# Optimization experiments

Hardware: AMD Instinct MI355X
Metric: run time of the kernel (lower is better)

## Reference

```python
import jax, jax.numpy as jnp
import numpy as np

B, N, C = 4, 8192, 512
H, Dh, G, R = 8, 64, 64, 2  # heads, dim_head, slice_num, mlp_ratio
EPS_LN = 1e-5
EPS_NORM = 1e-5


def _ln(x, g, b):
    m = jnp.mean(x, axis=-1, keepdims=True)
    v = jnp.var(x, axis=-1, keepdims=True)
    return (x - m) * jax.lax.rsqrt(v + EPS_LN) * g + b


def setup_inputs() -> dict:
    key = jax.random.key(0)
    ks = jax.random.split(key, 16)
    r = lambda k, shp: jax.random.normal(k, shp, jnp.float32) * 0.02
    inner = H * Dh
    return {
        "fx": jax.random.normal(ks[0], (B, N, C), jnp.float32),
        "ln1_g": jnp.ones((C,), jnp.float32), "ln1_b": jnp.zeros((C,), jnp.float32),
        "Wx": r(ks[1], (C, inner)), "bx": jnp.zeros((inner,), jnp.float32),
        "Wfx": r(ks[2], (C, inner)), "bfx": jnp.zeros((inner,), jnp.float32),
        "Wslice": r(ks[3], (Dh, G)), "bslice": jnp.zeros((G,), jnp.float32),
        "temperature": jnp.full((1, H, 1, 1), 0.5, jnp.float32),
        "Wq": r(ks[4], (Dh, Dh)), "Wk": r(ks[5], (Dh, Dh)), "Wv": r(ks[6], (Dh, Dh)),
        "Wout": r(ks[7], (inner, C)), "bout": jnp.zeros((C,), jnp.float32),
        "tln_g": jnp.ones((Dh,), jnp.float32), "tln_b": jnp.zeros((Dh,), jnp.float32),
        "Wm1": r(ks[8], (Dh, R * Dh)), "bm1": jnp.zeros((R * Dh,), jnp.float32),
        "Wm2": r(ks[9], (R * Dh, Dh)), "bm2": jnp.zeros((Dh,), jnp.float32),
    }


def reference(fx, ln1_g, ln1_b, Wx, bx, Wfx, bfx, Wslice, bslice, temperature,
              Wq, Wk, Wv, Wout, bout, tln_g, tln_b, Wm1, bm1, Wm2, bm2):
    fx_norm = _ln(fx, ln1_g, ln1_b)                          # [B,N,C]
    # _forward_slice: project to per-head mid features
    x_mid = (fx_norm @ Wx + bx).reshape(B, N, H, Dh).transpose(0, 2, 1, 3)   # [B,H,N,Dh]
    fx_mid = (fx_norm @ Wfx + bfx).reshape(B, N, H, Dh).transpose(0, 2, 1, 3)
    # _project_token: soft slice assignment + weighted pooling into G tokens
    logits = jnp.einsum('bhnd,dg->bhng', x_mid, Wslice) + bslice
    slice_w = jax.nn.softmax(logits / temperature, axis=-1)  # [B,H,N,G]
    slice_norm = jnp.sum(slice_w, axis=2)                    # [B,H,G]
    slice_tok = jnp.einsum('bhnd,bhng->bhgd', fx_mid, slice_w) / (slice_norm[..., None] + EPS_NORM)
    # attention over the small token set (G tokens)
    q = slice_tok @ Wq
    k = slice_tok @ Wk
    v = slice_tok @ Wv
    scale = Dh ** -0.5
    attn = jax.nn.softmax(jnp.einsum('bhgd,bhpd->bhgp', q, k) * scale, axis=-1)
    out_tok = jnp.einsum('bhgp,bhpd->bhgd', attn, v) + slice_tok
    # token MLP with residual
    h = _ln(out_tok, tln_g, tln_b)
    h = jax.nn.gelu(h @ Wm1 + bm1, approximate=False) @ Wm2 + bm2
    tokens = h + out_tok                                     # [B,H,G,Dh]
    # _deslice: weighted scatter back to N points, merge heads, out projection
    out_x = jnp.einsum('bhgd,bhng->bhnd', tokens, slice_w)
    out_x = out_x.transpose(0, 2, 1, 3).reshape(B, N, H * Dh)
    out = out_x @ Wout + bout
    return out + fx_norm
```

## Files before the change

### kernel.cpp

```cpp
#include <hip/hip_runtime.h>
#include <math.h>

#define B_ 4
#define N_ 8192
#define C_ 512
#define H_ 8
#define M_ (B_ * N_)

typedef __attribute__((ext_vector_type(8))) short bf16x8;
typedef __attribute__((ext_vector_type(4))) float f32x4;
typedef __attribute__((ext_vector_type(8))) unsigned short u16x8;
typedef __attribute__((ext_vector_type(4))) unsigned short u16x4;

__device__ __forceinline__ float b2f(unsigned short u) {
  union { unsigned int i; float f; } v;
  v.i = ((unsigned int)u) << 16;
  return v.f;
}
__device__ __forceinline__ unsigned short f2b(float f) {
  union { float f; unsigned int i; } v;
  v.f = f;
  unsigned int r = v.i + 0x7fff + ((v.i >> 16) & 1);
  return (unsigned short)(r >> 16);
}
__device__ __forceinline__ void gl_lds16(const void* g, void* l) {
  __builtin_amdgcn_global_load_lds(
      (const __attribute__((address_space(1))) unsigned int*)g,
      (__attribute__((address_space(3))) unsigned int*)l, 16, 0, 0);
}

__global__ __launch_bounds__(256) void ln_bf16(
    const float* __restrict__ x, const float* __restrict__ gam,
    const float* __restrict__ bet, unsigned short* __restrict__ y) {
  int wave = threadIdx.x >> 6, lane = threadIdx.x & 63;
  int row = (blockIdx.x << 2) + wave;
  const float4* xr = (const float4*)(x + (size_t)row * C_);
  float4 v0 = xr[lane], v1 = xr[lane + 64];
  float s = v0.x + v0.y + v0.z + v0.w + v1.x + v1.y + v1.z + v1.w;
  float q = v0.x * v0.x + v0.y * v0.y + v0.z * v0.z + v0.w * v0.w +
            v1.x * v1.x + v1.y * v1.y + v1.z * v1.z + v1.w * v1.w;
#pragma unroll
  for (int off = 32; off; off >>= 1) {
    s += __shfl_xor(s, off);
    q += __shfl_xor(q, off);
  }
  float mean = s * (1.0f / C_);
  float var = q * (1.0f / C_) - mean * mean;
  float rstd = rsqrtf(var + 1e-5f);
  const float4* gr = (const float4*)gam;
  const float4* br = (const float4*)bet;
  float4 g0 = gr[lane], g1 = gr[lane + 64];
  float4 b0 = br[lane], b1 = br[lane + 64];
  u16x4 oa, ob;
  oa.x = f2b((v0.x - mean) * rstd * g0.x + b0.x);
  oa.y = f2b((v0.y - mean) * rstd * g0.y + b0.y);
  oa.z = f2b((v0.z - mean) * rstd * g0.z + b0.z);
  oa.w = f2b((v0.w - mean) * rstd * g0.w + b0.w);
  ob.x = f2b((v1.x - mean) * rstd * g1.x + b1.x);
  ob.y = f2b((v1.y - mean) * rstd * g1.y + b1.y);
  ob.z = f2b((v1.z - mean) * rstd * g1.z + b1.z);
  ob.w = f2b((v1.w - mean) * rstd * g1.w + b1.w);
  unsigned short* yr = y + (size_t)row * C_;
  *(u16x4*)(yr + (lane << 2)) = oa;
  *(u16x4*)(yr + 256 + (lane << 2)) = ob;
}

__global__ __launch_bounds__(256) void prep_all(
    const float* __restrict__ Wx, const float* __restrict__ Wfx,
    const float* __restrict__ Wout, const float* __restrict__ Wsl,
    const float* __restrict__ Wq, const float* __restrict__ Wk,
    const float* __restrict__ Wv, const float* __restrict__ Wm1,
    const float* __restrict__ Wm2, unsigned short* __restrict__ WtX,
    unsigned short* __restrict__ WtF, unsigned short* __restrict__ WtO,
    unsigned short* __restrict__ wsf, unsigned short* __restrict__ wfr) {
  __shared__ float tile[64][65];
  int blk = blockIdx.x, t = threadIdx.x;
  if (blk < 192) {
    int which = blk >> 6, sub = blk & 63;
    const float* W = (which == 0) ? Wx : (which == 1) ? Wfx : Wout;
    unsigned short* Wt = (which == 0) ? WtX : (which == 1) ? WtF : WtO;
    int r0 = (sub >> 3) << 6, c0 = (sub & 7) << 6;
    int lr = t >> 4, lc = (t & 15) << 2;
#pragma unroll
    for (int p = 0; p < 4; p++) {
      float4 v = *(const float4*)(W + (size_t)(r0 + lr + p * 16) * 512 + c0 + lc);
      tile[lr + p * 16][lc + 0] = v.x;
      tile[lr + p * 16][lc + 1] = v.y;
      tile[lr + p * 16][lc + 2] = v.z;
      tile[lr + p * 16][lc + 3] = v.w;
    }
    __syncthreads();
    int on = t >> 2, ok = (t & 3) << 4;
    unsigned short tmp[16];
#pragma unroll
    for (int j = 0; j < 16; j++) tmp[j] = f2b(tile[ok + j][on]);
    unsigned short* op = Wt + (size_t)(c0 + on) * 512 + r0 + ok;
#pragma unroll
    for (int j4 = 0; j4 < 4; j4++)
      *(u16x4*)(op + (j4 << 2)) = *(u16x4*)(tmp + (j4 << 2));
  } else {
#pragma unroll
    for (int i = 0; i < 2; i++) {
      int idx = t + i * 256;
      int f = idx >> 6, l = idx & 63;
      int gt = f >> 1, ks = f & 1;
      int g = (gt << 4) + (l & 15);
      int d0 = (ks << 5) + ((l >> 4) << 3);
      unsigned short v[8];
#pragma unroll
      for (int jj = 0; jj < 8; jj++) v[jj] = f2b(Wsl[(size_t)(d0 + jj) * 64 + g]);
      *(u16x4*)(wsf + idx * 8) = *(u16x4*)v;
      *(u16x4*)(wsf + idx * 8 + 4) = *(u16x4*)(v + 4);
    }
    for (int task = t; task < 56 * 64; task += 256) {
      int fid = task >> 6, l = task & 63;
      const float* W;
      int stride, ct, ks;
      if (fid < 24) {
        W = (fid < 8) ? Wq : (fid < 16) ? Wk : Wv;
        int e = fid & 7;
        ct = e >> 1;
        ks = e & 1;
        stride = 64;
      } else if (fid < 40) {
        W = Wm1;
        int e = fid - 24;
        ct = e >> 1;
        ks = e & 1;
        stride = 128;
      } else {
        W = Wm2;
        int e = fid - 40;
        ct = e >> 2;
        ks = e & 3;
        stride = 64;
      }
      int d0 = (ks << 5) + ((l >> 4) << 3);
      int c = (ct << 4) + (l & 15);
      unsigned short v[8];
#pragma unroll
      for (int j = 0; j < 8; j++) v[j] = f2b(W[(size_t)(d0 + j) * stride + c]);
      *(u16x4*)(wfr + task * 8) = *(u16x4*)v;
      *(u16x4*)(wfr + task * 8 + 4) = *(u16x4*)(v + 4);
    }
  }
}

__global__ __launch_bounds__(256) void tokfrag_prep(
    const float* __restrict__ tokens, unsigned short* __restrict__ wtokf) {
  int bh = blockIdx.x, t = threadIdx.x, w = t >> 6, l = t & 63;
  const float* tp = tokens + ((size_t)bh << 12);
#pragma unroll
  for (int fid = w; fid < 8; fid += 4) {
    int mt = fid >> 1, ks = fid & 1;
    int d = (mt << 4) + (l & 15);
    int g0 = (ks << 5) + ((l >> 4) << 3);
    unsigned short v[8];
#pragma unroll
    for (int j = 0; j < 8; j++) v[j] = f2b(tp[(g0 + j) * 64 + d]);
    unsigned short* op = wtokf + (((size_t)bh << 3) + fid) * 512 + (l << 3);
    *(u16x4*)op = *(u16x4*)v;
    *(u16x4*)(op + 4) = *(u16x4*)(v + 4);
  }
}

template <int DEC, bool BIASROW, bool OUTBF, bool RES>
__global__ __launch_bounds__(256) void gemm_bf16(
    const unsigned short* __restrict__ A, const unsigned short* __restrict__ Bt,
    const float* __restrict__ bias, const unsigned short* __restrict__ resid,
    void* __restrict__ Cout, size_t ldC) {
  __shared__ unsigned short lds[8192];
  const int t = threadIdx.x;
  const int w = t >> 6, l = t & 63;
  int bid = blockIdx.x;
  int xcd = bid & 7, q = bid >> 3;
  int bm, bn;
  if (DEC == 0) {
    bm = ((xcd << 5) + (q >> 2)) << 7;
    bn = (q & 3) << 7;
  } else {
    bn = ((xcd << 5) + (q >> 2)) << 7;
    bm = (q & 3) << 7;
  }
  const int wm = (w >> 1) << 6, wn = (w & 1) << 6;
  f32x4 acc[4][4];
#pragma unroll
  for (int mt = 0; mt < 4; mt++)
#pragma unroll
    for (int nt = 0; nt < 4; nt++) acc[mt][nt] = (f32x4){0.f, 0.f, 0.f, 0.f};

  const int srow = t >> 2;
  const int scol = (((t & 3) ^ ((t >> 3) & 3)) << 3);
  const unsigned short* gA0 = A + (size_t)(bm + srow) * 512 + scol;
  const unsigned short* gA1 = A + (size_t)(bm + 64 + srow) * 512 + scol;
  const unsigned short* gB0 = Bt + (size_t)(bn + srow) * 512 + scol;
  const unsigned short* gB1 = Bt + (size_t)(bn + 64 + srow) * 512 + scol;
  const int fr = l & 15;
  const int pslot = (((l >> 4) ^ ((l >> 1) & 3)) << 3);

  for (int k0 = 0; k0 < 512; k0 += 32) {
    gl_lds16(gA0 + k0, lds + (w << 9));
    gl_lds16(gA1 + k0, lds + 2048 + (w << 9));
    gl_lds16(gB0 + k0, lds + 4096 + (w << 9));
    gl_lds16(gB1 + k0, lds + 6144 + (w << 9));
    __syncthreads();
    bf16x8 af[4], bfr[4];
#pragma unroll
    for (int mt = 0; mt < 4; mt++)
      af[mt] = *(const bf16x8*)&lds[(wm + mt * 16 + fr) * 32 + pslot];
#pragma unroll
    for (int nt = 0; nt < 4; nt++)
      bfr[nt] = *(const bf16x8*)&lds[4096 + (wn + nt * 16 + fr) * 32 + pslot];
#pragma unroll
    for (int mt = 0; mt < 4; mt++)
#pragma unroll
      for (int nt = 0; nt < 4; nt++)
        acc[mt][nt] = __builtin_amdgcn_mfma_f32_16x16x32_bf16(
            af[mt], bfr[nt], acc[mt][nt], 0, 0, 0);
    __syncthreads();
  }

  const int col0 = bn + wn + (l & 15);
  const int row0 = bm + wm + ((l >> 4) << 2);
#pragma unroll
  for (int mt = 0; mt < 4; mt++) {
#pragma unroll
    for (int j = 0; j < 4; j++) {
      int row = row0 + mt * 16 + j;
#pragma unroll
      for (int nt = 0; nt < 4; nt++) {
        int col = col0 + nt * 16;
        float v = acc[mt][nt][j] + (BIASROW ? bias[row] : bias[col]);
        if (RES) v += b2f(resid[(size_t)row * ldC + col]);
        if (OUTBF)
          ((unsigned short*)Cout)[(size_t)row * ldC + col] = f2b(v);
        else
          ((float*)Cout)[(size_t)row * ldC + col] = v;
      }
    }
  }
}

__global__ __launch_bounds__(256) void slice_mfma(
    unsigned short* __restrict__ xw, const unsigned short* __restrict__ wf,
    const float* __restrict__ bslice, const float* __restrict__ temp) {
  __shared__ unsigned short xs[4096];
  int t = threadIdx.x, w = t >> 6, l = t & 63;
  int blk = blockIdx.x;
  size_t base = (size_t)blk << 12;
  {
    int srow = t >> 2;
    const unsigned short* gp = xw + base + srow * 64 + ((t & 3) << 4);
    u16x8 a = *(const u16x8*)gp;
    u16x8 b = *(const u16x8*)(gp + 8);
    int sl0 = (t & 3) << 1, swz = srow & 7;
    *(u16x8*)&xs[srow * 64 + ((sl0 ^ swz) << 3)] = a;
    *(u16x8*)&xs[srow * 64 + (((sl0 + 1) ^ swz) << 3)] = b;
  }
  bf16x8 wsf[4][2];
#pragma unroll
  for (int gt = 0; gt < 4; gt++)
#pragma unroll
    for (int ks = 0; ks < 2; ks++)
      wsf[gt][ks] = *(const bf16x8*)(wf + (((gt << 1) + ks) * 64 + l) * 8);
  __syncthreads();

  int xr = (w << 4) + (l & 15);
  f32x4 acc[4];
#pragma unroll
  for (int gt = 0; gt < 4; gt++) acc[gt] = (f32x4){0.f, 0.f, 0.f, 0.f};
#pragma unroll
  for (int ks = 0; ks < 2; ks++) {
    int slot = (ks << 2) + (l >> 4);
    bf16x8 xf = *(const bf16x8*)&xs[xr * 64 + ((slot ^ (xr & 7)) << 3)];
#pragma unroll
    for (int gt = 0; gt < 4; gt++)
      acc[gt] = __builtin_amdgcn_mfma_f32_16x16x32_bf16(wsf[gt][ks], xf,
                                                        acc[gt], 0, 0, 0);
  }

  int gxr = (blk << 6) + xr;
  float invt = 1.0f / temp[gxr & 7];
  int qq = l >> 4;
  float lg[16];
  float mx = -1e30f;
#pragma unroll
  for (int gt = 0; gt < 4; gt++)
#pragma unroll
    for (int r = 0; r < 4; r++) {
      float v = (acc[gt][r] + bslice[(gt << 4) + (qq << 2) + r]) * invt;
      lg[(gt << 2) + r] = v;
      mx = fmaxf(mx, v);
    }
  mx = fmaxf(mx, __shfl_xor(mx, 16));
  mx = fmaxf(mx, __shfl_xor(mx, 32));
  float ssum = 0.f;
#pragma unroll
  for (int i = 0; i < 16; i++) {
    lg[i] = expf(lg[i] - mx);
    ssum += lg[i];
  }
  ssum += __shfl_xor(ssum, 16);
  ssum += __shfl_xor(ssum, 32);
  float inv = 1.0f / ssum;
  __syncthreads();
#pragma unroll
  for (int gt = 0; gt < 4; gt++) {
    int slot = (gt << 1) + (qq >> 1);
    int off = ((slot ^ (xr & 7)) << 3) + ((qq & 1) << 2);
    u16x4 pk;
    pk.x = f2b(lg[(gt << 2) + 0] * inv);
    pk.y = f2b(lg[(gt << 2) + 1] * inv);
    pk.z = f2b(lg[(gt << 2) + 2] * inv);
    pk.w = f2b(lg[(gt << 2) + 3] * inv);
    *(u16x4*)&xs[xr * 64 + off] = pk;
  }
  __syncthreads();
  {
    int rr = (w << 4) + (l >> 2);
    int sl = (l & 3) << 1, swz = rr & 7;
    u16x8 o0 = *(const u16x8*)&xs[rr * 64 + ((sl ^ swz) << 3)];
    u16x8 o1 = *(const u16x8*)&xs[rr * 64 + (((sl + 1) ^ swz) << 3)];
    unsigned short* op = xw + base + rr * 64 + ((l & 3) << 4);
    *(u16x8*)op = o0;
    *(u16x8*)(op + 8) = o1;
  }
}

__global__ __launch_bounds__(256) void pool_mfma(
    const unsigned short* __restrict__ sw, const unsigned short* __restrict__ fxT,
    float* __restrict__ tok_part, float* __restrict__ norm_part) {
  __shared__ unsigned short wT[4096];
  int bid = blockIdx.x;
  int bh = bid >> 4, c = bid & 15;
  int b = bh >> 3, h = bh & 7;
  int t = threadIdx.x, w = t >> 6, l = t & 63;
  int n0 = c << 9;
  const int fr15 = l & 15, fs = l >> 4;
  f32x4 acc[4];
#pragma unroll
  for (int gt = 0; gt < 4; gt++) acc[gt] = (f32x4){0.f, 0.f, 0.f, 0.f};
  float nacc[4] = {0.f, 0.f, 0.f, 0.f};

  const unsigned short* fxrow =
      fxT + (size_t)(h * 64 + w * 16 + fr15) * 32768 + b * N_ + n0 + (fs << 3);

  for (int nn = 0; nn < 512; nn += 64) {
    size_t srow = ((size_t)(b * N_ + n0 + nn + l) * 8 + h) << 6;
    u16x8 a0 = *(const u16x8*)(sw + srow + w * 16);
    u16x8 a1 = *(const u16x8*)(sw + srow + w * 16 + 8);
    __syncthreads();
#pragma unroll
    for (int j = 0; j < 16; j++) {
      int g = (w << 4) + j;
      unsigned short v = (j < 8) ? (unsigned short)a0[j] : (unsigned short)a1[j - 8];
      wT[(g << 6) + (((l >> 3) ^ (g & 7)) << 3) + (l & 7)] = v;
    }
    __syncthreads();
#pragma unroll
    for (int kk = 0; kk < 2; kk++) {
      bf16x8 bfrag = *(const bf16x8*)(fxrow + nn + (kk << 5));
#pragma unroll
      for (int gt = 0; gt < 4; gt++) {
        int g = (gt << 4) + fr15;
        int slot = (kk << 2) + fs;
        bf16x8 af = *(const bf16x8*)&wT[(g << 6) + ((slot ^ (g & 7)) << 3)];
        acc[gt] = __builtin_amdgcn_mfma_f32_16x16x32_bf16(af, bfrag, acc[gt], 0, 0, 0);
        if (w == 0) {
#pragma unroll
          for (int j = 0; j < 8; j++) nacc[gt] += b2f((unsigned short)af[j]);
        }
      }
    }
  }
  float* op = tok_part + ((size_t)bid << 12);
#pragma unroll
  for (int gt = 0; gt < 4; gt++)
#pragma unroll
    for (int rr = 0; rr < 4; rr++)
      op[((gt << 4) + (fs << 2) + rr) * 64 + (w << 4) + fr15] = acc[gt][rr];
  if (w == 0) {
#pragma unroll
    for (int gt = 0; gt < 4; gt++) {
      float s = nacc[gt];
      s += __shfl_xor(s, 16);
      s += __shfl_xor(s, 32);
      if (l < 16) norm_part[(bid << 6) + (gt << 4) + l] = s;
    }
  }
}

__global__ __launch_bounds__(256) void tok_reduce(
    const float* __restrict__ tok_part, const float* __restrict__ norm_part,
    float* __restrict__ stG) {
  int blk = blockIdx.x;
  int bh = blk >> 2, qq = blk & 3;
  int t = threadIdx.x;
  int e = (qq << 10) + (t << 2);
  int g = e >> 6;
  float s = 0.f;
  const float* np = norm_part + ((size_t)bh << 10);
#pragma unroll
  for (int c = 0; c < 16; c++) s += np[(c << 6) + g];
  float4 acc = make_float4(0.f, 0.f, 0.f, 0.f);
  const float* tp = tok_part + ((size_t)bh << 16) + e;
#pragma unroll
  for (int c = 0; c < 16; c++) {
    float4 v = *(const float4*)(tp + (c << 12));
    acc.x += v.x;
    acc.y += v.y;
    acc.z += v.z;
    acc.w += v.w;
  }
  float inv = 1.0f / (s + 1e-5f);
  acc.x *= inv;
  acc.y *= inv;
  acc.z *= inv;
  acc.w *= inv;
  *(float4*)(stG + ((size_t)bh << 12) + e) = acc;
}

__device__ __forceinline__ float gelu_exact(float x) {
  return 0.5f * x * (1.0f + erff(x * 0.70710678118654752f));
}

__global__ __launch_bounds__(256) void token_mfma(
    const float* __restrict__ stG, const unsigned short* __restrict__ wfr,
    const float* __restrict__ tg, const float* __restrict__ tb,
    const float* __restrict__ bm1, const float* __restrict__ bm2,
    float* __restrict__ tokens) {
  __shared__ __align__(16) char smem[54272];
  unsigned short* stb = (unsigned short*)smem;
  float* st32 = (float*)(smem + 9216);
  unsigned short* hmld = (unsigned short*)(smem + 9216);
  unsigned short* qld = (unsigned short*)(smem + 26624);
  unsigned short* kld = (unsigned short*)(smem + 35840);
  unsigned short* vtl = (unsigned short*)(smem + 45056);

  int bh = blockIdx.x, t = threadIdx.x, w = t >> 6, l = t & 63;
  const int fr = l & 15, fq = l >> 4;

  {
    int r = t >> 2, c0 = (t & 3) << 4;
    const float* gp = stG + ((size_t)bh << 12) + r * 64 + c0;
    float4 a = *(const float4*)gp;
    float4 b = *(const float4*)(gp + 4);
    float4 c = *(const float4*)(gp + 8);
    float4 d = *(const float4*)(gp + 12);
    *(float4*)&st32[r * 68 + c0] = a;
    *(float4*)&st32[r * 68 + c0 + 4] = b;
    *(float4*)&st32[r * 68 + c0 + 8] = c;
    *(float4*)&st32[r * 68 + c0 + 12] = d;
    unsigned short tv[16];
    tv[0] = f2b(a.x); tv[1] = f2b(a.y); tv[2] = f2b(a.z); tv[3] = f2b(a.w);
    tv[4] = f2b(b.x); tv[5] = f2b(b.y); tv[6] = f2b(b.z); tv[7] = f2b(b.w);
    tv[8] = f2b(c.x); tv[9] = f2b(c.y); tv[10] = f2b(c.z); tv[11] = f2b(c.w);
    tv[12] = f2b(d.x); tv[13] = f2b(d.y); tv[14] = f2b(d.z); tv[15] = f2b(d.w);
    *(u16x8*)&stb[r * 72 + c0] = *(u16x8*)tv;
    *(u16x8*)&stb[r * 72 + c0 + 8] = *(u16x8*)(tv + 8);
  }
  __syncthreads();

  const int orow = (w << 4) + (fq << 2);

  {
    bf16x8 af[2];
#pragma unroll
    for (int ks = 0; ks < 2; ks++)
      af[ks] = *(const bf16x8*)&stb[((w << 4) + fr) * 72 + (ks << 5) + (fq << 3)];
    f32x4 aq[4], ak[4], av[4];
#pragma unroll
    for (int ct = 0; ct < 4; ct++) {
      aq[ct] = (f32x4){0.f, 0.f, 0.f, 0.f};
      ak[ct] = (f32x4){0.f, 0.f, 0.f, 0.f};
      av[ct] = (f32x4){0.f, 0.f, 0.f, 0.f};
    }
#pragma unroll
    for (int ct = 0; ct < 4; ct++)
#pragma unroll
      for (int ks = 0; ks < 2; ks++) {
        bf16x8 bq = *(const bf16x8*)&wfr[(((ct << 1) + ks) * 64 + l) * 8];
        aq[ct] = __builtin_amdgcn_mfma_f32_16x16x32_bf16(af[ks], bq, aq[ct], 0, 0, 0);
      }
#pragma unroll
    for (int ct = 0; ct < 4; ct++)
#pragma unroll
      for (int ks = 0; ks < 2; ks++) {
        bf16x8 bk = *(const bf16x8*)&wfr[((8 + (ct << 1) + ks) * 64 + l) * 8];
        ak[ct] = __builtin_amdgcn_mfma_f32_16x16x32_bf16(af[ks], bk, ak[ct], 0, 0, 0);
      }
#pragma unroll
    for (int ct = 0; ct < 4; ct++)
#pragma unroll
      for (int ks = 0; ks < 2; ks++) {
        bf16x8 bv = *(const bf16x8*)&wfr[((16 + (ct << 1) + ks) * 64 + l) * 8];
        av[ct] = __builtin_amdgcn_mfma_f32_16x16x32_bf16(af[ks], bv, av[ct], 0, 0, 0);
      }
#pragma unroll
    for (int ct = 0; ct < 4; ct++) {
#pragma unroll
      for (int rr = 0; rr < 4; rr++) {
        qld[(orow + rr) * 72 + (ct << 4) + fr] = f2b(aq[ct][rr]);
        kld[(orow + rr) * 72 + (ct << 4) + fr] = f2b(ak[ct][rr]);
      }
      u16x4 vp;
      vp.x = f2b(av[ct][0]);
      vp.y = f2b(av[ct][1]);
      vp.z = f2b(av[ct][2]);
      vp.w = f2b(av[ct][3]);
      *(u16x4*)&vtl[((ct << 4) + fr) * 72 + orow] = vp;
    }
  }
  __syncthreads();

  {
    bf16x8 aq[2];
#pragma unroll
    for (int ks = 0; ks < 2; ks++)
      aq[ks] = *(const bf16x8*)&qld[((w << 4) + fr) * 72 + (ks << 5) + (fq << 3)];
    f32x4 accs[4];
#pragma unroll
    for (int nt = 0; nt < 4; nt++) accs[nt] = (f32x4){0.f, 0.f, 0.f, 0.f};
#pragma unroll
    for (int nt = 0; nt < 4; nt++)
#pragma unroll
      for (int ks = 0; ks < 2; ks++) {
        bf16x8 bk = *(const bf16x8*)&kld[((nt << 4) + fr) * 72 + (ks << 5) + (fq << 3)];
        accs[nt] = __builtin_amdgcn_mfma_f32_16x16x32_bf16(aq[ks], bk, accs[nt], 0, 0, 0);
      }
#pragma unroll
    for (int rr = 0; rr < 4; rr++) {
      float v0 = accs[0][rr] * 0.125f, v1 = accs[1][rr] * 0.125f;
      float v2 = accs[2][rr] * 0.125f, v3 = accs[3][rr] * 0.125f;
      float mx = fmaxf(fmaxf(v0, v1), fmaxf(v2, v3));
      mx = fmaxf(mx, __shfl_xor(mx, 1));
      mx = fmaxf(mx, __shfl_xor(mx, 2));
      mx = fmaxf(mx, __shfl_xor(mx, 4));
      mx = fmaxf(mx, __shfl_xor(mx, 8));
      float e0 = expf(v0 - mx), e1 = expf(v1 - mx);
      float e2 = expf(v2 - mx), e3 = expf(v3 - mx);
      float ss = e0 + e1 + e2 + e3;
      ss += __shfl_xor(ss, 1);
      ss += __shfl_xor(ss, 2);
      ss += __shfl_xor(ss, 4);
      ss += __shfl_xor(ss, 8);
      float inv = 1.0f / ss;
      stb[(orow + rr) * 72 + 0 * 16 + fr] = f2b(e0 * inv);
      stb[(orow + rr) * 72 + 1 * 16 + fr] = f2b(e1 * inv);
      stb[(orow + rr) * 72 + 2 * 16 + fr] = f2b(e2 * inv);
      stb[(orow + rr) * 72 + 3 * 16 + fr] = f2b(e3 * inv);
    }
  }
  __syncthreads();

  float o16[4][4];
  {
    bf16x8 ap[2];
#pragma unroll
    for (int ks = 0; ks < 2; ks++)
      ap[ks] = *(const bf16x8*)&stb[((w << 4) + fr) * 72 + (ks << 5) + (fq << 3)];
    f32x4 acco[4];
#pragma unroll
    for (int ct = 0; ct < 4; ct++) acco[ct] = (f32x4){0.f, 0.f, 0.f, 0.f};
#pragma unroll
    for (int ct = 0; ct < 4; ct++)
#pragma unroll
      for (int ks = 0; ks < 2; ks++) {
        bf16x8 bv = *(const bf16x8*)&vtl[((ct << 4) + fr) * 72 + (ks << 5) + (fq << 3)];
        acco[ct] = __builtin_amdgcn_mfma_f32_16x16x32_bf16(ap[ks], bv, acco[ct], 0, 0, 0);
      }
    float tgv[4], tbv[4];
#pragma unroll
    for (int ct = 0; ct < 4; ct++) {
      tgv[ct] = tg[(ct << 4) + fr];
      tbv[ct] = tb[(ct << 4) + fr];
    }
#pragma unroll
    for (int ct = 0; ct < 4; ct++)
#pragma unroll
      for (int rr = 0; rr < 4; rr++)
        o16[ct][rr] = acco[ct][rr] + st32[(orow + rr) * 68 + (ct << 4) + fr];
#pragma unroll
    for (int rr = 0; rr < 4; rr++) {
      float sm = o16[0][rr] + o16[1][rr] + o16[2][rr] + o16[3][rr];
      float sq = o16[0][rr] * o16[0][rr] + o16[1][rr] * o16[1][rr] +
                 o16[2][rr] * o16[2][rr] + o16[3][rr] * o16[3][rr];
      sm += __shfl_xor(sm, 1);
      sm += __shfl_xor(sm, 2);
      sm += __shfl_xor(sm, 4);
      sm += __shfl_xor(sm, 8);
      sq += __shfl_xor(sq, 1);
      sq += __shfl_xor(sq, 2);
      sq += __shfl_xor(sq, 4);
      sq += __shfl_xor(sq, 8);
      float mean = sm * (1.0f / 64.0f);
      float var = sq * (1.0f / 64.0f) - mean * mean;
      float rstd = rsqrtf(var + 1e-5f);
#pragma unroll
      for (int ct = 0; ct < 4; ct++) {
        float hv = (o16[ct][rr] - mean) * rstd * tgv[ct] + tbv[ct];
        qld[(orow + rr) * 72 + (ct << 4) + fr] = f2b(hv);
      }
    }
  }
  __syncthreads();

  {
    bf16x8 ah[2];
#pragma unroll
    for (int ks = 0; ks < 2; ks++)
      ah[ks] = *(const bf16x8*)&qld[((w << 4) + fr) * 72 + (ks << 5) + (fq << 3)];
    f32x4 accm[8];
#pragma unroll
    for (int et = 0; et < 8; et++) accm[et] = (f32x4){0.f, 0.f, 0.f, 0.f};
#pragma unroll
    for (int et = 0; et < 8; et++)
#pragma unroll
      for (int ks = 0; ks < 2; ks++) {
        bf16x8 bm = *(const bf16x8*)&wfr[((24 + (et << 1) + ks) * 64 + l) * 8];
        accm[et] = __builtin_amdgcn_mfma_f32_16x16x32_bf16(ah[ks], bm, accm[et], 0, 0, 0);
      }
#pragma unroll
    for (int et = 0; et < 8; et++) {
      float bv = bm1[(et << 4) + fr];
#pragma unroll
      for (int rr = 0; rr < 4; rr++) {
        float x = accm[et][rr] + bv;
        hmld[(orow + rr) * 136 + (et << 4) + fr] = f2b(gelu_exact(x));
      }
    }
  }
  __syncthreads();

  {
    bf16x8 ahm[4];
#pragma unroll
    for (int ks = 0; ks < 4; ks++)
      ahm[ks] = *(const bf16x8*)&hmld[((w << 4) + fr) * 136 + (ks << 5) + (fq << 3)];
    f32x4 acc2[4];
#pragma unroll
    for (int ct = 0; ct < 4; ct++) acc2[ct] = (f32x4){0.f, 0.f, 0.f, 0.f};
#pragma unroll
    for (int ct = 0; ct < 4; ct++)
#pragma unroll
      for (int ks = 0; ks < 4; ks++) {
        bf16x8 bw = *(const bf16x8*)&wfr[((40 + (ct << 2) + ks) * 64 + l) * 8];
        acc2[ct] = __builtin_amdgcn_mfma_f32_16x16x32_bf16(ahm[ks], bw, acc2[ct], 0, 0, 0);
      }
    float* tout = tokens + ((size_t)bh << 12);
#pragma unroll
    for (int ct = 0; ct < 4; ct++) {
      float bv = bm2[(ct << 4) + fr];
#pragma unroll
      for (int rr = 0; rr < 4; rr++)
        tout[(orow + rr) * 64 + (ct << 4) + fr] = acc2[ct][rr] + bv + o16[ct][rr];
    }
  }
}

__global__ __launch_bounds__(256) void deslice_mfma(
    const unsigned short* __restrict__ wtokf, const unsigned short* __restrict__ sw,
    unsigned short* __restrict__ outx) {
  int bid = blockIdx.x;
  int bh = bid >> 4, c = bid & 15;
  int b = bh >> 3, h = bh & 7;
  int t = threadIdx.x, w = t >> 6, l = t & 63;
  const int fr = l & 15, fq = l >> 4;

  bf16x8 ta[4][2];
  const unsigned short* fp = wtokf + ((size_t)bh << 12);
#pragma unroll
  for (int mt = 0; mt < 4; mt++)
#pragma unroll
    for (int ks = 0; ks < 2; ks++)
      ta[mt][ks] = *(const bf16x8*)(fp + (((mt << 1) + ks) << 9) + (l << 3));

  int n0 = (c << 9) + (w << 7);
#pragma unroll 2
  for (int ntile = 0; ntile < 8; ntile++) {
    int nb = n0 + (ntile << 4);
    size_t rowb = ((size_t)(b * N_ + nb + fr) * 8 + h) << 6;
    bf16x8 b0 = *(const bf16x8*)(sw + rowb + (fq << 3));
    bf16x8 b1 = *(const bf16x8*)(sw + rowb + 32 + (fq << 3));
    f32x4 acc[4];
#pragma unroll
    for (int mt = 0; mt < 4; mt++) acc[mt] = (f32x4){0.f, 0.f, 0.f, 0.f};
#pragma unroll
    for (int mt = 0; mt < 4; mt++) {
      acc[mt] = __builtin_amdgcn_mfma_f32_16x16x32_bf16(ta[mt][0], b0, acc[mt], 0, 0, 0);
      acc[mt] = __builtin_amdgcn_mfma_f32_16x16x32_bf16(ta[mt][1], b1, acc[mt], 0, 0, 0);
    }
    unsigned short* op = outx + rowb + (fq << 2);
#pragma unroll
    for (int mt = 0; mt < 4; mt++) {
      u16x4 pk;
      pk.x = f2b(acc[mt][0]);
      pk.y = f2b(acc[mt][1]);
      pk.z = f2b(acc[mt][2]);
      pk.w = f2b(acc[mt][3]);
      *(u16x4*)(op + (mt << 4)) = pk;
    }
  }
}

extern "C" void kernel_launch(void* const* d_in, const int* in_sizes, int n_in,
                              void* d_out, int out_size, void* d_ws,
                              size_t ws_size, hipStream_t stream) {
  const float* fx = (const float*)d_in[0];
  const float* ln1g = (const float*)d_in[1];
  const float* ln1b = (const float*)d_in[2];
  const float* Wx = (const float*)d_in[3];
  const float* bx = (const float*)d_in[4];
  const float* Wfx = (const float*)d_in[5];
  const float* bfx = (const float*)d_in[6];
  const float* Wsl = (const float*)d_in[7];
  const float* bsl = (const float*)d_in[8];
  const float* temp = (const float*)d_in[9];
  const float* Wq = (const float*)d_in[10];
  const float* Wk = (const float*)d_in[11];
  const float* Wv = (const float*)d_in[12];
  const float* Wout = (const float*)d_in[13];
  const float* bout = (const float*)d_in[14];
  const float* tlng = (const float*)d_in[15];
  const float* tlnb = (const float*)d_in[16];
  const float* Wm1 = (const float*)d_in[17];
  const float* bm1 = (const float*)d_in[18];
  const float* Wm2 = (const float*)d_in[19];
  const float* bm2 = (const float*)d_in[20];
  float* out = (float*)d_out;

  char* p = (char*)d_ws;
  const size_t MC2 = (size_t)M_ * 512 * 2;
  unsigned short* fxn = (unsigned short*)p;  p += MC2;
  unsigned short* buf1 = (unsigned short*)p; p += MC2;
  unsigned short* bufT = (unsigned short*)p; p += MC2;
  unsigned short* WtX = (unsigned short*)p;  p += 512 * 512 * 2;
  unsigned short* WtF = (unsigned short*)p;  p += 512 * 512 * 2;
  unsigned short* WtO = (unsigned short*)p;  p += 512 * 512 * 2;
  unsigned short* wsf = (unsigned short*)p;  p += 8192;
  unsigned short* wfr = (unsigned short*)p;  p += 56 * 512 * 2;
  unsigned short* wtokf = (unsigned short*)p; p += (size_t)32 * 8 * 512 * 2;
  float* tok_part = (float*)p;  p += (size_t)512 * 4096 * 4;
  float* norm_part = (float*)p; p += (size_t)512 * 64 * 4;
  float* tokens = (float*)p;    p += (size_t)32 * 4096 * 4;
  float* stG = (float*)p;       p += (size_t)32 * 4096 * 4;

  ln_bf16<<<M_ / 4, 256, 0, stream>>>(fx, ln1g, ln1b, fxn);
  prep_all<<<193, 256, 0, stream>>>(Wx, Wfx, Wout, Wsl, Wq, Wk, Wv, Wm1, Wm2,
                                    WtX, WtF, WtO, wsf, wfr);
  gemm_bf16<0, false, true, false><<<1024, 256, 0, stream>>>(fxn, WtX, bx, nullptr, buf1, 512);
  gemm_bf16<1, true, true, false><<<1024, 256, 0, stream>>>(WtF, fxn, bfx, nullptr, bufT, 32768);
  slice_mfma<<<4096, 256, 0, stream>>>(buf1, wsf, bsl, temp);
  pool_mfma<<<512, 256, 0, stream>>>(buf1, bufT, tok_part, norm_part);
  tok_reduce<<<128, 256, 0, stream>>>(tok_part, norm_part, stG);
  token_mfma<<<32, 256, 0, stream>>>(stG, wfr, tlng, tlnb, bm1, bm2, tokens);
  tokfrag_prep<<<32, 256, 0, stream>>>(tokens, wtokf);
  deslice_mfma<<<512, 256, 0, stream>>>(wtokf, buf1, bufT);
  gemm_bf16<0, false, false, true><<<1024, 256, 0, stream>>>(bufT, WtO, bout, fxn, out, 512);
}
```

Measured before the change: 185.3 us.

## Deepen GEMM K-tile to 64 and fuse token fragment prep into token kernel

The bf16 GEMM now stages a 64-wide K slice per iteration, using 32KB of LDS with an 8-way XOR swizzle. This halves the number of barrier pairs and the load/sync overhead across the three big projections. Separately, token_mfma now writes its output straight into the bf16 MFMA fragment layout through LDS, which removes the tokfrag_prep launch and the fp32 tokens round trip. The larger LDS footprint may reduce occupancy of the GEMM blocks.

```diff
diff --git a/kernel.cpp b/kernel.cpp
--- a/kernel.cpp
+++ b/kernel.cpp
@@ -146,30 +146,12 @@
   }
 }
 
-__global__ __launch_bounds__(256) void tokfrag_prep(
-    const float* __restrict__ tokens, unsigned short* __restrict__ wtokf) {
-  int bh = blockIdx.x, t = threadIdx.x, w = t >> 6, l = t & 63;
-  const float* tp = tokens + ((size_t)bh << 12);
-#pragma unroll
-  for (int fid = w; fid < 8; fid += 4) {
-    int mt = fid >> 1, ks = fid & 1;
-    int d = (mt << 4) + (l & 15);
-    int g0 = (ks << 5) + ((l >> 4) << 3);
-    unsigned short v[8];
-#pragma unroll
-    for (int j = 0; j < 8; j++) v[j] = f2b(tp[(g0 + j) * 64 + d]);
-    unsigned short* op = wtokf + (((size_t)bh << 3) + fid) * 512 + (l << 3);
-    *(u16x4*)op = *(u16x4*)v;
-    *(u16x4*)(op + 4) = *(u16x4*)(v + 4);
-  }
-}
-
 template <int DEC, bool BIASROW, bool OUTBF, bool RES>
 __global__ __launch_bounds__(256) void gemm_bf16(
     const unsigned short* __restrict__ A, const unsigned short* __restrict__ Bt,
     const float* __restrict__ bias, const unsigned short* __restrict__ resid,
     void* __restrict__ Cout, size_t ldC) {
-  __shared__ unsigned short lds[8192];
+  __shared__ unsigned short lds[16384];
   const int t = threadIdx.x;
   const int w = t >> 6, l = t & 63;
   int bid = blockIdx.x;
@@ -189,34 +171,40 @@
 #pragma unroll
     for (int nt = 0; nt < 4; nt++) acc[mt][nt] = (f32x4){0.f, 0.f, 0.f, 0.f};
 
-  const int srow = t >> 2;
-  const int scol = (((t & 3) ^ ((t >> 3) & 3)) << 3);
-  const unsigned short* gA0 = A + (size_t)(bm + srow) * 512 + scol;
-  const unsigned short* gA1 = A + (size_t)(bm + 64 + srow) * 512 + scol;
-  const unsigned short* gB0 = Bt + (size_t)(bn + srow) * 512 + scol;
-  const unsigned short* gB1 = Bt + (size_t)(bn + 64 + srow) * 512 + scol;
-  const int fr = l & 15;
-  const int pslot = (((l >> 4) ^ ((l >> 1) & 3)) << 3);
-
-  for (int k0 = 0; k0 < 512; k0 += 32) {
-    gl_lds16(gA0 + k0, lds + (w << 9));
-    gl_lds16(gA1 + k0, lds + 2048 + (w << 9));
-    gl_lds16(gB0 + k0, lds + 4096 + (w << 9));
-    gl_lds16(gB1 + k0, lds + 6144 + (w << 9));
+  const int srow = t >> 3;
+  const int scol = (((t & 7) ^ ((t >> 3) & 7)) << 3);
+  const unsigned short* gA = A + (size_t)(bm + srow) * 512 + scol;
+  const unsigned short* gB = Bt + (size_t)(bn + srow) * 512 + scol;
+  const int fr = l & 15, qq = l >> 4;
+
+  for (int k0 = 0; k0 < 512; k0 += 64) {
+#pragma unroll
+    for (int i = 0; i < 4; i++)
+      gl_lds16(gA + (size_t)(i << 5) * 512 + k0, lds + (i << 11) + (w << 9));
+#pragma unroll
+    for (int i = 0; i < 4; i++)
+      gl_lds16(gB + (size_t)(i << 5) * 512 + k0, lds + 8192 + (i << 11) + (w << 9));
     __syncthreads();
-    bf16x8 af[4], bfr[4];
-#pragma unroll
-    for (int mt = 0; mt < 4; mt++)
-      af[mt] = *(const bf16x8*)&lds[(wm + mt * 16 + fr) * 32 + pslot];
-#pragma unroll
-    for (int nt = 0; nt < 4; nt++)
-      bfr[nt] = *(const bf16x8*)&lds[4096 + (wn + nt * 16 + fr) * 32 + pslot];
-#pragma unroll
-    for (int mt = 0; mt < 4; mt++)
-#pragma unroll
-      for (int nt = 0; nt < 4; nt++)
-        acc[mt][nt] = __builtin_amdgcn_mfma_f32_16x16x32_bf16(
-            af[mt], bfr[nt], acc[mt][nt], 0, 0, 0);
+#pragma unroll
+    for (int kk = 0; kk < 2; kk++) {
+      bf16x8 af[4], bfr[4];
+#pragma unroll
+      for (int mt = 0; mt < 4; mt++) {
+        int row = wm + mt * 16 + fr;
+        af[mt] = *(const bf16x8*)&lds[row * 64 + ((((kk << 2) + qq) ^ (fr & 7)) << 3)];
+      }
+#pragma unroll
+      for (int nt = 0; nt < 4; nt++) {
+        int row = wn + nt * 16 + fr;
+        bfr[nt] = *(const bf16x8*)&lds[8192 + row * 64 + ((((kk << 2) + qq) ^ (fr & 7)) << 3)];
+      }
+#pragma unroll
+      for (int mt = 0; mt < 4; mt++)
+#pragma unroll
+        for (int nt = 0; nt < 4; nt++)
+          acc[mt][nt] = __builtin_amdgcn_mfma_f32_16x16x32_bf16(
+              af[mt], bfr[nt], acc[mt][nt], 0, 0, 0);
+    }
     __syncthreads();
   }
 
@@ -428,7 +416,7 @@
     const float* __restrict__ stG, const unsigned short* __restrict__ wfr,
     const float* __restrict__ tg, const float* __restrict__ tb,
     const float* __restrict__ bm1, const float* __restrict__ bm2,
-    float* __restrict__ tokens) {
+    unsigned short* __restrict__ wtokf) {
   __shared__ __align__(16) char smem[54272];
   unsigned short* stb = (unsigned short*)smem;
   float* st32 = (float*)(smem + 9216);
@@ -647,13 +635,28 @@
         bf16x8 bw = *(const bf16x8*)&wfr[((40 + (ct << 2) + ks) * 64 + l) * 8];
         acc2[ct] = __builtin_amdgcn_mfma_f32_16x16x32_bf16(ahm[ks], bw, acc2[ct], 0, 0, 0);
       }
-    float* tout = tokens + ((size_t)bh << 12);
 #pragma unroll
     for (int ct = 0; ct < 4; ct++) {
       float bv = bm2[(ct << 4) + fr];
 #pragma unroll
       for (int rr = 0; rr < 4; rr++)
-        tout[(orow + rr) * 64 + (ct << 4) + fr] = acc2[ct][rr] + bv + o16[ct][rr];
+        stb[(orow + rr) * 72 + (ct << 4) + fr] =
+            f2b(acc2[ct][rr] + bv + o16[ct][rr]);
+    }
+  }
+  __syncthreads();
+  {
+#pragma unroll
+    for (int e = 0; e < 2; e++) {
+      int fid = (w << 1) + e;
+      int d = (w << 4) + (l & 15);
+      int g0 = (e << 5) + ((l >> 4) << 3);
+      unsigned short v[8];
+#pragma unroll
+      for (int j = 0; j < 8; j++) v[j] = stb[(g0 + j) * 72 + d];
+      unsigned short* op = wtokf + (((size_t)bh << 3) + fid) * 512 + (l << 3);
+      *(u16x4*)op = *(u16x4*)v;
+      *(u16x4*)(op + 4) = *(u16x4*)(v + 4);
     }
   }
 }
@@ -742,7 +745,6 @@
   unsigned short* wtokf = (unsigned short*)p; p += (size_t)32 * 8 * 512 * 2;
   float* tok_part = (float*)p;  p += (size_t)512 * 4096 * 4;
   float* norm_part = (float*)p; p += (size_t)512 * 64 * 4;
-  float* tokens = (float*)p;    p += (size_t)32 * 4096 * 4;
   float* stG = (float*)p;       p += (size_t)32 * 4096 * 4;
 
   ln_bf16<<<M_ / 4, 256, 0, stream>>>(fx, ln1g, ln1b, fxn);
@@ -753,8 +755,7 @@
   slice_mfma<<<4096, 256, 0, stream>>>(buf1, wsf, bsl, temp);
   pool_mfma<<<512, 256, 0, stream>>>(buf1, bufT, tok_part, norm_part);
   tok_reduce<<<128, 256, 0, stream>>>(tok_part, norm_part, stG);
-  token_mfma<<<32, 256, 0, stream>>>(stG, wfr, tlng, tlnb, bm1, bm2, tokens);
-  tokfrag_prep<<<32, 256, 0, stream>>>(tokens, wtokf);
+  token_mfma<<<32, 256, 0, stream>>>(stG, wfr, tlng, tlnb, bm1, bm2, wtokf);
   deslice_mfma<<<512, 256, 0, stream>>>(wtokf, buf1, bufT);
   gemm_bf16<0, false, false, true><<<1024, 256, 0, stream>>>(bufT, WtO, bout, fxn, out, 512);
 }
```

Result: faster. 172.5 us (-6.9%).
